# Kernel tuning notes

Hardware: AMD Instinct MI355X
Metric: run time of the kernel (lower is better)

The kernel has to match this reference:

```python
import jax, jax.numpy as jnp
import numpy as np

B, D, LD, LP = 8, 192, 128, 1024
FC = [1024, 1024, 512]
NC = 2


def setup_inputs() -> dict:
    key = jax.random.key(0)
    ks = jax.random.split(key, 18)
    s = 0.05  # small init scale for numerical sanity
    inp = {
        "drug_conv": jax.random.normal(ks[0], (B, D, LD), jnp.float32),
        "protein_conv": jax.random.normal(ks[1], (B, D, LP), jnp.float32),
        "Wd": jax.random.normal(ks[2], (D, D), jnp.float32) * s,
        "bd": jax.random.normal(ks[3], (D,), jnp.float32) * s,
        "Wp": jax.random.normal(ks[4], (D, D), jnp.float32) * s,
        "bp": jax.random.normal(ks[5], (D,), jnp.float32) * s,
        "Wa": jax.random.normal(ks[6], (D, D), jnp.float32) * s,
        "ba": jax.random.normal(ks[7], (D,), jnp.float32) * s,
        "W1": jax.random.normal(ks[8], (FC[0], 2 * D), jnp.float32) * s,
        "b1": jax.random.normal(ks[9], (FC[0],), jnp.float32) * s,
        "W2": jax.random.normal(ks[10], (FC[1], FC[0]), jnp.float32) * s,
        "b2": jax.random.normal(ks[11], (FC[1],), jnp.float32) * s,
        "W3": jax.random.normal(ks[12], (FC[2], FC[1]), jnp.float32) * s,
        "b3": jax.random.normal(ks[13], (FC[2],), jnp.float32) * s,
        "Wo": jax.random.normal(ks[14], (NC, FC[2]), jnp.float32) * s,
        "bo": jax.random.normal(ks[15], (NC,), jnp.float32) * s,
    }
    return inp


def reference(drug_conv, protein_conv, Wd, bd, Wp, bp, Wa, ba,
              W1, b1, W2, b2, W3, b3, Wo, bo):
    # drug_conv: (B, D, Ld); protein_conv: (B, D, Lp). Torch Linear: y = x @ W.T + b
    d_att = jnp.einsum('bdl,ed->ble', drug_conv, Wd) + bd      # (B, Ld, D)
    p_att = jnp.einsum('bdl,ed->ble', protein_conv, Wp) + bp   # (B, Lp, D)
    # broadcast additive cross-attention: (B, Ld, Lp, D)
    h = jax.nn.relu(d_att[:, :, None, :] + p_att[:, None, :, :])
    A = jnp.einsum('blpd,ed->blpe', h, Wa) + ba                # (B, Ld, Lp, D)
    comp_att = jax.nn.sigmoid(jnp.mean(A, axis=2))             # (B, Ld, D)
    prot_att = jax.nn.sigmoid(jnp.mean(A, axis=1))             # (B, Lp, D)
    # gated residual: x*0.5 + x*att  (att permuted back to (B, D, L))
    drug = drug_conv * (0.5 + jnp.transpose(comp_att, (0, 2, 1)))
    prot = protein_conv * (0.5 + jnp.transpose(prot_att, (0, 2, 1)))
    # MaxPool1d over full sequence length == max along last axis
    drug_pooled = jnp.max(drug, axis=2)                        # (B, D)
    prot_pooled = jnp.max(prot, axis=2)                        # (B, D)
    pair = jnp.concatenate([drug_pooled, prot_pooled], axis=1) # (B, 2D)
    lrelu = lambda x: jax.nn.leaky_relu(x, 0.01)
    h1 = lrelu(pair @ W1.T + b1)
    h2 = lrelu(h1 @ W2.T + b2)
    h3 = lrelu(h2 @ W3.T + b3)
    return h3 @ Wo.T + bo                                      # (B, num_classes)
```

## Files before the change

### kernel.cpp

```cpp
#include <hip/hip_runtime.h>
#include <math.h>

#define BB 8
#define DD 192
#define LLD 128
#define LLP 1024
#define FC1 1024
#define FC2 1024
#define FC3 512
#define NCLS 2
#define LT 8

__device__ __forceinline__ void atomicMaxFloat(float* addr, float value) {
    if (value >= 0.f) atomicMax((int*)addr, __float_as_int(value));
    else atomicMin((unsigned int*)addr, __float_as_uint(value));
}

__global__ void proj_both_kernel(const float* __restrict__ drug,
                                 const float* __restrict__ prot,
                                 const float* __restrict__ Wd,
                                 const float* __restrict__ bdv,
                                 const float* __restrict__ Wp,
                                 const float* __restrict__ bpv,
                                 float* __restrict__ d_att_t,
                                 float* __restrict__ p_att_t) {
    int blk = blockIdx.x;
    int tid = threadIdx.x;

    const float *x, *W, *bias;
    float* y;
    int L, b, l0;
    if (blk < BB * (LLD / LT)) {
        x = drug; W = Wd; bias = bdv; y = d_att_t; L = LLD;
        b = blk >> 4; l0 = (blk & 15) * LT;
    } else {
        int idx = blk - BB * (LLD / LT);
        x = prot; W = Wp; bias = bpv; y = p_att_t; L = LLP;
        b = idx >> 7; l0 = (idx & 127) * LT;
    }

    __shared__ float xs[LT][DD + 4];

    const float* xbase = x + (size_t)b * DD * L + l0;
#pragma unroll
    for (int k = 0; k < LT; ++k) {
        int idx = tid + k * DD;
        int d = idx >> 3;
        int j = idx & (LT - 1);
        xs[j][d] = xbase[(size_t)d * L + j];
    }
    __syncthreads();

    const int e = tid;
    const float be = bias[e];
    float acc[LT];
#pragma unroll
    for (int j = 0; j < LT; ++j) acc[j] = be;

    const float4* Wr4 = (const float4*)(W + (size_t)e * DD);
#pragma unroll 2
    for (int d4 = 0; d4 < DD / 4; ++d4) {
        float4 w = Wr4[d4];
#pragma unroll
        for (int j = 0; j < LT; ++j) {
            float4 h = *(const float4*)&xs[j][d4 * 4];
            acc[j] = fmaf(h.x, w.x, acc[j]);
            acc[j] = fmaf(h.y, w.y, acc[j]);
            acc[j] = fmaf(h.z, w.z, acc[j]);
            acc[j] = fmaf(h.w, w.w, acc[j]);
        }
    }

    float* ybase = y + ((size_t)b * DD + e) * L + l0;
    *(float4*)&ybase[0] = make_float4(acc[0], acc[1], acc[2], acc[3]);
    *(float4*)&ybase[4] = make_float4(acc[4], acc[5], acc[6], acc[7]);
}

__global__ void cross_sort_kernel(const float* __restrict__ da_t,
                                  const float* __restrict__ pa_t,
                                  float* __restrict__ Hd_t,
                                  float* __restrict__ Hp_t,
                                  float* __restrict__ pair) {
    int blk = blockIdx.x;
    int b = blk / (DD / 2);
    int dp = blk - b * (DD / 2);
    int d0 = dp * 2;
    int tid = threadIdx.x;
    int wave = tid >> 6, lane = tid & 63;

    __shared__ float skey[2][LLD];
    __shared__ float sufs[2][LLD + 1];
    __shared__ int   cnt[2][LLD + 1];
    __shared__ float val[2][LLD + 1];

    float s0 = 0.f, s1 = 0.f;
    int i0 = 0, i1 = 0;

    if (wave < 2) {
        const int a = wave;
        const float* base = da_t + ((size_t)b * DD + d0 + a) * LLD;
        s0 = base[lane];
        s1 = base[lane + 64];
        i0 = lane; i1 = lane + 64;

        for (int k = 2; k <= LLD; k <<= 1) {
            for (int j = k >> 1; j > 0; j >>= 1) {
                if (j == 64) {
                    if (s0 > s1) {
                        float tk = s0; s0 = s1; s1 = tk;
                        int ti = i0; i0 = i1; i1 = ti;
                    }
                } else {
                    {
                        float pk = __shfl_xor(s0, j);
                        int   pi = __shfl_xor(i0, j);
                        bool keep_min = (((lane & k) == 0) == ((lane & j) == 0));
                        bool take = keep_min ? (pk < s0) : (pk > s0);
                        if (take) { s0 = pk; i0 = pi; }
                    }
                    {
                        int e = lane | 64;
                        float pk = __shfl_xor(s1, j);
                        int   pi = __shfl_xor(i1, j);
                        bool keep_min = (((e & k) == 0) == ((e & j) == 0));
                        bool take = keep_min ? (pk < s1) : (pk > s1);
                        if (take) { s1 = pk; i1 = pi; }
                    }
                }
            }
        }

        float t1 = s1;
#pragma unroll
        for (int off = 1; off < 64; off <<= 1) {
            int src = lane + off;
            float v = __shfl(t1, src & 63);
            t1 += (src < 64) ? v : 0.f;
        }
        float tot1 = __shfl(t1, 0);
        float t0 = s0;
#pragma unroll
        for (int off = 1; off < 64; off <<= 1) {
            int src = lane + off;
            float v = __shfl(t0, src & 63);
            t0 += (src < 64) ? v : 0.f;
        }

        skey[a][lane] = s0;
        skey[a][lane + 64] = s1;
        sufs[a][lane] = t0 + tot1;
        sufs[a][lane + 64] = t1;
        if (lane == 0) sufs[a][LLD] = 0.f;
    } else if (wave == 2) {
        for (int i = lane; i < 2 * (LLD + 1); i += 64) ((int*)cnt)[i] = 0;
        if (lane < 4) {
            int side = lane >> 1;
            pair[b * 2 * DD + side * DD + d0 + (lane & 1)] = -INFINITY;
        }
    } else {
        for (int i = lane; i < 2 * (LLD + 1); i += 64) ((float*)val)[i] = 0.f;
    }
    __syncthreads();

    {
        int d_i = tid & 1, prow = tid >> 1;
        float* hprow = Hp_t + ((size_t)b * DD + d0 + d_i) * LLP;
        const float* qbase = pa_t + ((size_t)b * DD + d0 + d_i) * LLP;
#pragma unroll
        for (int batch = 0; batch < LLP / 128; ++batch) {
            int p = batch * 128 + prow;
            float q = qbase[p];
            float nq = -q;
            int pos = 0;
#pragma unroll
            for (int st = LLD; st > 0; st >>= 1) {
                int np = pos + st;
                if (np <= LLD && skey[d_i][np - 1] <= nq) pos = np;
            }
            hprow[p] = ((float)(LLD - pos) * q + sufs[d_i][pos]) * (1.0f / LLD);
            atomicAdd(&cnt[d_i][pos], 1);
            atomicAdd(&val[d_i][pos], q);
        }
    }
    __syncthreads();

    if (wave < 2) {
        const int a = wave;
        int   c0 = cnt[a][lane], c1 = cnt[a][lane + 64];
        float v0 = val[a][lane], v1 = val[a][lane + 64];
#pragma unroll
        for (int off = 1; off < 64; off <<= 1) {
            int src = lane - off;
            int   cu = __shfl(c0, src & 63);
            float vu = __shfl(v0, src & 63);
            if (src >= 0) { c0 += cu; v0 += vu; }
        }
        int   ct0 = __shfl(c0, 63);
        float vt0 = __shfl(v0, 63);
#pragma unroll
        for (int off = 1; off < 64; off <<= 1) {
            int src = lane - off;
            int   cu = __shfl(c1, src & 63);
            float vu = __shfl(v1, src & 63);
            if (src >= 0) { c1 += cu; v1 += vu; }
        }
        c1 += ct0; v1 += vt0;

        float* hdrow = Hd_t + ((size_t)b * DD + d0 + a) * LLD;
        hdrow[i0] = (s0 * (float)c0 + v0) * (1.0f / LLP);
        hdrow[i1] = (s1 * (float)c1 + v1) * (1.0f / LLP);
    }
}

__global__ void gemm_sig_pool_kernel(const float* __restrict__ Hd_t,
                                     const float* __restrict__ Hp_t,
                                     const float* __restrict__ Wa,
                                     const float* __restrict__ ba,
                                     const float* __restrict__ drug,
                                     const float* __restrict__ prot,
                                     float* __restrict__ pair) {
    int blk = blockIdx.x;
    const float* Ht;
    const float* xsrc;
    int L, b, l0, side;
    if (blk < BB * (LLD / LT)) {
        b = blk >> 4; l0 = (blk & 15) * LT;
        Ht = Hd_t; xsrc = drug; L = LLD; side = 0;
    } else {
        int idx = blk - BB * (LLD / LT);
        b = idx >> 7; l0 = (idx & 127) * LT;
        Ht = Hp_t; xsrc = prot; L = LLP; side = 1;
    }
    int tid = threadIdx.x;

    __shared__ float hs[LT][DD + 4];

    const float* hrow = Ht + ((size_t)b * DD + tid) * L + l0;
#pragma unroll
    for (int j = 0; j < LT; ++j) hs[j][tid] = hrow[j];
    __syncthreads();

    const int e = tid;
    const float bias = ba[e];
    float acc[LT];
#pragma unroll
    for (int j = 0; j < LT; ++j) acc[j] = bias;

    const float4* Wr4 = (const float4*)(Wa + (size_t)e * DD);
#pragma unroll 2
    for (int d4 = 0; d4 < DD / 4; ++d4) {
        float4 w = Wr4[d4];
#pragma unroll
        for (int j = 0; j < LT; ++j) {
            float4 h = *(const float4*)&hs[j][d4 * 4];
            acc[j] = fmaf(h.x, w.x, acc[j]);
            acc[j] = fmaf(h.y, w.y, acc[j]);
            acc[j] = fmaf(h.z, w.z, acc[j]);
            acc[j] = fmaf(h.w, w.w, acc[j]);
        }
    }

    const float* xrow = xsrc + ((size_t)b * DD + e) * L + l0;
    float4 x0 = *(const float4*)&xrow[0];
    float4 x1 = *(const float4*)&xrow[4];
    float xv[LT] = {x0.x, x0.y, x0.z, x0.w, x1.x, x1.y, x1.z, x1.w};
    float m = -INFINITY;
#pragma unroll
    for (int j = 0; j < LT; ++j) {
        float gate = 0.5f + 1.0f / (1.0f + __expf(-acc[j]));
        m = fmaxf(m, xv[j] * gate);
    }
    atomicMaxFloat(&pair[b * 2 * DD + side * DD + e], m);
}

__global__ void fc_wave_kernel(const float* __restrict__ x,
                               const float* __restrict__ W,
                               const float* __restrict__ bias,
                               float* __restrict__ y,
                               int K, int N, int leaky) {
    int gtid = blockIdx.x * blockDim.x + threadIdx.x;
    int wid = gtid >> 6;
    int lane = gtid & 63;
    if (wid >= BB * N) return;
    int b = wid / N;
    int j = wid - b * N;
    const float4* xr = (const float4*)(x + (size_t)b * K);
    const float4* Wr = (const float4*)(W + (size_t)j * K);
    int K4 = K >> 2;
    float s = 0.f;
    for (int k = lane; k < K4; k += 64) {
        float4 xv = xr[k];
        float4 wv = Wr[k];
        s = fmaf(xv.x, wv.x, s);
        s = fmaf(xv.y, wv.y, s);
        s = fmaf(xv.z, wv.z, s);
        s = fmaf(xv.w, wv.w, s);
    }
#pragma unroll
    for (int off = 32; off > 0; off >>= 1) s += __shfl_xor(s, off);
    if (lane == 0) {
        float acc = s + bias[j];
        if (leaky) acc = (acc > 0.f) ? acc : 0.01f * acc;
        y[wid] = acc;
    }
}

extern "C" void kernel_launch(void* const* d_in, const int* in_sizes, int n_in,
                              void* d_out, int out_size, void* d_ws, size_t ws_size,
                              hipStream_t stream) {
    const float* drug = (const float*)d_in[0];
    const float* prot = (const float*)d_in[1];
    const float* Wd = (const float*)d_in[2];
    const float* bd = (const float*)d_in[3];
    const float* Wp = (const float*)d_in[4];
    const float* bp = (const float*)d_in[5];
    const float* Wa = (const float*)d_in[6];
    const float* ba = (const float*)d_in[7];
    const float* W1 = (const float*)d_in[8];
    const float* b1 = (const float*)d_in[9];
    const float* W2 = (const float*)d_in[10];
    const float* b2 = (const float*)d_in[11];
    const float* W3 = (const float*)d_in[12];
    const float* b3 = (const float*)d_in[13];
    const float* Wo = (const float*)d_in[14];
    const float* bo = (const float*)d_in[15];
    float* out = (float*)d_out;

    float* ws = (float*)d_ws;
    const size_t n_datt = (size_t)BB * LLD * DD;
    const size_t n_patt = (size_t)BB * LLP * DD;
    float* d_att_t = ws;
    float* p_att_t = d_att_t + n_datt;
    float* Hd_t    = p_att_t + n_patt;
    float* Hp_t    = Hd_t + n_datt;
    float* pair    = Hp_t + n_patt;
    float* h1      = pair + (size_t)BB * 2 * DD;
    float* h2      = h1 + (size_t)BB * FC1;
    float* h3      = h2 + (size_t)BB * FC2;

    proj_both_kernel<<<BB * (LLD / LT) + BB * (LLP / LT), DD, 0, stream>>>(
        drug, prot, Wd, bd, Wp, bp, d_att_t, p_att_t);

    cross_sort_kernel<<<BB * (DD / 2), 256, 0, stream>>>(
        d_att_t, p_att_t, Hd_t, Hp_t, pair);

    gemm_sig_pool_kernel<<<BB * (LLD / LT) + BB * (LLP / LT), DD, 0, stream>>>(
        Hd_t, Hp_t, Wa, ba, drug, prot, pair);

    fc_wave_kernel<<<(BB * FC1 * 64) / 256, 256, 0, stream>>>(pair, W1, b1, h1, 2 * DD, FC1, 1);
    fc_wave_kernel<<<(BB * FC2 * 64) / 256, 256, 0, stream>>>(h1, W2, b2, h2, FC1, FC2, 1);
    fc_wave_kernel<<<(BB * FC3 * 64) / 256, 256, 0, stream>>>(h2, W3, b3, h3, FC2, FC3, 1);
    fc_wave_kernel<<<(BB * NCLS * 64 + 255) / 256, 256, 0, stream>>>(h3, Wo, bo, out, FC3, NCLS, 0);
}
```

Measured before the change: 96.67 us.

## Fuse four MLP layers into one per-batch kernel with shared-memory activations

```diff
diff --git a/kernel.cpp b/kernel.cpp
--- a/kernel.cpp
+++ b/kernel.cpp
@@ -273,35 +273,73 @@
     atomicMaxFloat(&pair[b * 2 * DD + side * DD + e], m);
 }
 
-__global__ void fc_wave_kernel(const float* __restrict__ x,
-                               const float* __restrict__ W,
-                               const float* __restrict__ bias,
-                               float* __restrict__ y,
-                               int K, int N, int leaky) {
-    int gtid = blockIdx.x * blockDim.x + threadIdx.x;
-    int wid = gtid >> 6;
-    int lane = gtid & 63;
-    if (wid >= BB * N) return;
-    int b = wid / N;
-    int j = wid - b * N;
-    const float4* xr = (const float4*)(x + (size_t)b * K);
-    const float4* Wr = (const float4*)(W + (size_t)j * K);
+__device__ __forceinline__ void mlp_layer(const float* __restrict__ W,
+                                          const float* __restrict__ bias,
+                                          const float* __restrict__ xin,
+                                          float* __restrict__ xout,
+                                          int K, int N, int leaky,
+                                          int wid, int lane) {
     int K4 = K >> 2;
-    float s = 0.f;
-    for (int k = lane; k < K4; k += 64) {
-        float4 xv = xr[k];
-        float4 wv = Wr[k];
-        s = fmaf(xv.x, wv.x, s);
-        s = fmaf(xv.y, wv.y, s);
-        s = fmaf(xv.z, wv.z, s);
-        s = fmaf(xv.w, wv.w, s);
-    }
-#pragma unroll
-    for (int off = 32; off > 0; off >>= 1) s += __shfl_xor(s, off);
-    if (lane == 0) {
-        float acc = s + bias[j];
-        if (leaky) acc = (acc > 0.f) ? acc : 0.01f * acc;
-        y[wid] = acc;
+    for (int j = wid; j < N; j += 16) {
+        const float4* Wr = (const float4*)(W + (size_t)j * K);
+        float s = 0.f;
+        for (int k = lane; k < K4; k += 64) {
+            float4 wv = Wr[k];
+            float4 xv = *(const float4*)&xin[k * 4];
+            s = fmaf(xv.x, wv.x, s);
+            s = fmaf(xv.y, wv.y, s);
+            s = fmaf(xv.z, wv.z, s);
+            s = fmaf(xv.w, wv.w, s);
+        }
+#pragma unroll
+        for (int off = 32; off > 0; off >>= 1) s += __shfl_xor(s, off);
+        if (lane == 0) {
+            float acc = s + bias[j];
+            xout[j] = leaky ? ((acc > 0.f) ? acc : 0.01f * acc) : acc;
+        }
+    }
+}
+
+__global__ void __launch_bounds__(1024) mlp_kernel(
+        const float* __restrict__ pair,
+        const float* __restrict__ W1, const float* __restrict__ b1,
+        const float* __restrict__ W2, const float* __restrict__ b2,
+        const float* __restrict__ W3, const float* __restrict__ b3,
+        const float* __restrict__ Wo, const float* __restrict__ bo,
+        float* __restrict__ out) {
+    int b = blockIdx.x;
+    int tid = threadIdx.x;
+    int wid = tid >> 6, lane = tid & 63;
+
+    __shared__ float xa[FC1];
+    __shared__ float xb[FC1];
+
+    if (tid < 2 * DD) xa[tid] = pair[b * 2 * DD + tid];
+    __syncthreads();
+
+    mlp_layer(W1, b1, xa, xb, 2 * DD, FC1, 1, wid, lane);
+    __syncthreads();
+    mlp_layer(W2, b2, xb, xa, FC1, FC2, 1, wid, lane);
+    __syncthreads();
+    mlp_layer(W3, b3, xa, xb, FC2, FC3, 1, wid, lane);
+    __syncthreads();
+    {
+        int K4 = FC3 >> 2;
+        for (int j = wid; j < NCLS; j += 16) {
+            const float4* Wr = (const float4*)(Wo + (size_t)j * FC3);
+            float s = 0.f;
+            for (int k = lane; k < K4; k += 64) {
+                float4 wv = Wr[k];
+                float4 xv = *(const float4*)&xb[k * 4];
+                s = fmaf(xv.x, wv.x, s);
+                s = fmaf(xv.y, wv.y, s);
+                s = fmaf(xv.z, wv.z, s);
+                s = fmaf(xv.w, wv.w, s);
+            }
+#pragma unroll
+            for (int off = 32; off > 0; off >>= 1) s += __shfl_xor(s, off);
+            if (lane == 0) out[b * NCLS + j] = s + bo[j];
+        }
     }
 }
 
@@ -334,9 +372,6 @@
     float* Hd_t    = p_att_t + n_patt;
     float* Hp_t    = Hd_t + n_datt;
     float* pair    = Hp_t + n_patt;
-    float* h1      = pair + (size_t)BB * 2 * DD;
-    float* h2      = h1 + (size_t)BB * FC1;
-    float* h3      = h2 + (size_t)BB * FC2;
 
     proj_both_kernel<<<BB * (LLD / LT) + BB * (LLP / LT), DD, 0, stream>>>(
         drug, prot, Wd, bd, Wp, bp, d_att_t, p_att_t);
@@ -347,8 +382,6 @@
     gemm_sig_pool_kernel<<<BB * (LLD / LT) + BB * (LLP / LT), DD, 0, stream>>>(
         Hd_t, Hp_t, Wa, ba, drug, prot, pair);
 
-    fc_wave_kernel<<<(BB * FC1 * 64) / 256, 256, 0, stream>>>(pair, W1, b1, h1, 2 * DD, FC1, 1);
-    fc_wave_kernel<<<(BB * FC2 * 64) / 256, 256, 0, stream>>>(h1, W2, b2, h2, FC1, FC2, 1);
-    fc_wave_kernel<<<(BB * FC3 * 64) / 256, 256, 0, stream>>>(h2, W3, b3, h3, FC2, FC3, 1);
-    fc_wave_kernel<<<(BB * NCLS * 64 + 255) / 256, 256, 0, stream>>>(h3, Wo, bo, out, FC3, NCLS, 0);
-}
+    mlp_kernel<<<BB, 1024, 0, stream>>>(pair, W1, b1, W2, b2, W3, b3,
+                                        Wo, bo, out);
+}
```

New measurement: 325.3 us. 3.37x slower.
